# Kernel optimization log

Measured on AMD Instinct MI355X. Metric: run time of the kernel, lower is better.

Reference implementation:

```python
import jax, jax.numpy as jnp
import numpy as np

B, S, H = 512, 100, 768
LAMB = 0.8

def setup_inputs() -> dict:
    key = jax.random.key(0)
    k1, k2, k3, k4 = jax.random.split(key, 4)
    scale = 1.0 / np.sqrt(H)
    return {
        "sent_vec": jax.random.normal(k1, (B, S, H), dtype=jnp.float32),
        "mask_cls": jnp.ones((B, S), dtype=jnp.int32),
        "W_cont": jax.random.normal(k2, (1, H), dtype=jnp.float32) * scale,
        "W_sim": jax.random.normal(k3, (H, H), dtype=jnp.float32) * scale,
        "W_rel": jax.random.normal(k4, (H, H), dtype=jnp.float32) * scale,
        "b_matrix": jnp.zeros((1, 1), dtype=jnp.float32),
    }

def reference(sent_vec, mask_cls, W_cont, W_sim, W_rel, b_matrix):
    # sent_vec: [B,S,H], mask_cls: [B,S] (all ones -> true_dim == S)
    m = mask_cls.astype(sent_vec.dtype)                       # [B,S]
    mask2 = m[:, :, None] * m[:, None, :]                     # mask_my_own [B,S,S]

    # Score_Cont[b,i,j] = W_cont . sent_vec[b,i]
    cont = jnp.einsum('h,bih->bi', W_cont[0], sent_vec)       # [B,S]
    # Score_Sim[b,i,j] = sent_i W_sim sent_j^T, masked
    sim = jnp.einsum('bih,hk,bjk->bij', sent_vec, W_sim, sent_vec) * mask2
    # Score_rel[b,i,j] = sent_i W_rel d_rep, masked
    d_rep = sent_vec.mean(axis=1)                             # [B,H]
    rel = jnp.einsum('bih,hk,bk->bi', sent_vec, W_rel, d_rep) # [B,S]

    q = jax.nn.sigmoid(rel[:, :, None] * mask2 + cont[:, :, None] + sim + b_matrix[0, 0])
    q = q * mask2                                             # [B,S,S]

    # D = diag(column sums of q); q @ D^{-1} divides columns by sum_vec
    sum_vec = q.sum(axis=1)                                   # [B,S]
    qD = q / sum_vec[:, None, :]                              # [B,S,S]

    I = jnp.eye(S, dtype=q.dtype)
    M = I[None, :, :] - LAMB * qD                             # [B,S,S]
    y = jnp.full((B, S, 1), 1.0 / S, dtype=q.dtype)
    # Final_score = (1-lamb) * inv(I - lamb q D^-1) @ y  (solve == inverse@mm)
    score = (1.0 - LAMB) * jnp.linalg.solve(M, y)[:, :, 0]    # [B,S]
    return score
```

## Files before the change

### kernel.cpp

```cpp
#include <hip/hip_runtime.h>
#include <math.h>

#define BB 512
#define SS 100
#define HH 768

typedef __bf16 bf16x8 __attribute__((ext_vector_type(8)));
typedef __bf16 bf16x4 __attribute__((ext_vector_type(4)));
typedef float f32x4 __attribute__((ext_vector_type(4)));
typedef float f32x16 __attribute__((ext_vector_type(16)));

__device__ __forceinline__ void gld16(const void* g, void* l) {
    __builtin_amdgcn_global_load_lds((const __attribute__((address_space(1))) char*)g,
                                     (__attribute__((address_space(3))) char*)l, 16, 0, 0);
}

__global__ __launch_bounds__(256) void k_drep(const float* __restrict__ X,
                                              float* __restrict__ drep) {
    int b = blockIdx.x, g = blockIdx.y;
    int lane = threadIdx.x & 63, w = threadIdx.x >> 6;
    const float4* xb = (const float4*)(X + (size_t)b * SS * HH);
    int c4 = g * 64 + lane;
    float4 s = {0.f, 0.f, 0.f, 0.f};
    for (int r = w; r < SS; r += 4) {
        float4 v = xb[r * 192 + c4];
        s.x += v.x; s.y += v.y; s.z += v.z; s.w += v.w;
    }
    __shared__ float4 red[4][64];
    red[w][lane] = s;
    __syncthreads();
    if (w == 0) {
        float4 a0 = red[0][lane], a1 = red[1][lane], a2 = red[2][lane], a3 = red[3][lane];
        float4 o;
        o.x = (a0.x + a1.x + a2.x + a3.x) * (1.0f / SS);
        o.y = (a0.y + a1.y + a2.y + a3.y) * (1.0f / SS);
        o.z = (a0.z + a1.z + a2.z + a3.z) * (1.0f / SS);
        o.w = (a0.w + a1.w + a2.w + a3.w) * (1.0f / SS);
        ((float4*)(drep + (size_t)b * HH))[c4] = o;
    }
}

__global__ __launch_bounds__(256) void k_gemm_nt(const float* __restrict__ A,
                                                 const float* __restrict__ Bm,
                                                 float* __restrict__ C,
                                                 int N, int K) {
    __shared__ float As[64 * 20];
    __shared__ float Bs[64 * 20];
    int tid = threadIdx.x;
    int ty = tid >> 4, tx = tid & 15;
    int m0 = blockIdx.y * 64, n0 = blockIdx.x * 64;
    int lr = tid >> 2, lc = (tid & 3) * 4;
    float acc[4][4] = {};
    for (int kt = 0; kt < K; kt += 16) {
        *(float4*)(As + lr * 20 + lc) = *(const float4*)(A + (size_t)(m0 + lr) * K + kt + lc);
        *(float4*)(Bs + lr * 20 + lc) = *(const float4*)(Bm + (size_t)(n0 + lr) * K + kt + lc);
        __syncthreads();
        #pragma unroll
        for (int k = 0; k < 16; k += 2) {
            float2 ar[4], br[4];
            #pragma unroll
            for (int ii = 0; ii < 4; ++ii) ar[ii] = *(const float2*)(As + (ty + 16 * ii) * 20 + k);
            #pragma unroll
            for (int jj = 0; jj < 4; ++jj) br[jj] = *(const float2*)(Bs + (tx + 16 * jj) * 20 + k);
            #pragma unroll
            for (int ii = 0; ii < 4; ++ii)
                #pragma unroll
                for (int jj = 0; jj < 4; ++jj)
                    acc[ii][jj] = fmaf(ar[ii].y, br[jj].y, fmaf(ar[ii].x, br[jj].x, acc[ii][jj]));
        }
        __syncthreads();
    }
    #pragma unroll
    for (int ii = 0; ii < 4; ++ii)
        #pragma unroll
        for (int jj = 0; jj < 4; ++jj)
            C[(size_t)(m0 + ty + 16 * ii) * N + n0 + tx + 16 * jj] = acc[ii][jj];
}

__global__ __launch_bounds__(256) void k_splitw(const float* __restrict__ W,
                                                __bf16* __restrict__ th,
                                                __bf16* __restrict__ tl) {
    __shared__ float tile[32][33];
    int bn = blockIdx.x * 32, bk = blockIdx.y * 32;
    int tx = threadIdx.x & 31, ty = threadIdx.x >> 5;
    for (int r = ty; r < 32; r += 8)
        tile[r][tx] = W[(size_t)(bk + r) * HH + bn + tx];
    __syncthreads();
    for (int r = ty; r < 32; r += 8) {
        float v = tile[tx][r];
        __bf16 hv = (__bf16)v;
        size_t idx = (size_t)(bn + r) * HH + bk + tx;
        th[idx] = hv;
        tl[idx] = (__bf16)(v - (float)hv);
    }
}

__global__ __launch_bounds__(512) void k_split_contrel(const float* __restrict__ X,
                                                       const float* __restrict__ Wc,
                                                       const float* __restrict__ tmat,
                                                       const float* __restrict__ bmat,
                                                       __bf16* __restrict__ Xh,
                                                       __bf16* __restrict__ Xl,
                                                       float* __restrict__ avec,
                                                       int b_off) {
    __shared__ float4 u4[192];
    int lb = blockIdx.x, half = blockIdx.y;
    int b = b_off + lb;
    int tid = threadIdx.x, lane = tid & 63, w = tid >> 6;
    for (int c = tid; c < 192; c += 512) {
        float4 wc = ((const float4*)Wc)[c];
        float4 tm = ((const float4*)(tmat + (size_t)b * HH))[c];
        float4 o = {wc.x + tm.x, wc.y + tm.y, wc.z + tm.z, wc.w + tm.w};
        u4[c] = o;
    }
    __syncthreads();
    float b00 = bmat[0];
    const float4* xb = (const float4*)(X + (size_t)b * SS * HH);
    bf16x4* xh4 = (bf16x4*)(Xh + (size_t)lb * SS * HH);
    bf16x4* xl4 = (bf16x4*)(Xl + (size_t)lb * SS * HH);
    int rend = half * 50 + 50;
    for (int r = half * 50 + w; r < rend; r += 8) {
        float s = 0.f;
        #pragma unroll
        for (int cc = 0; cc < 3; ++cc) {
            int c = cc * 64 + lane;
            float4 v = xb[r * 192 + c];
            float4 uu = u4[c];
            s = fmaf(v.x, uu.x, fmaf(v.y, uu.y, fmaf(v.z, uu.z, fmaf(v.w, uu.w, s))));
            bf16x4 hv, lv;
            hv[0] = (__bf16)v.x; lv[0] = (__bf16)(v.x - (float)hv[0]);
            hv[1] = (__bf16)v.y; lv[1] = (__bf16)(v.y - (float)hv[1]);
            hv[2] = (__bf16)v.z; lv[2] = (__bf16)(v.z - (float)hv[2]);
            hv[3] = (__bf16)v.w; lv[3] = (__bf16)(v.w - (float)hv[3]);
            xh4[r * 192 + c] = hv;
            xl4[r * 192 + c] = lv;
        }
        #pragma unroll
        for (int off = 32; off > 0; off >>= 1) s += __shfl_down(s, off);
        if (lane == 0) avec[(size_t)b * SS + r] = s + b00;
    }
}

__global__ __launch_bounds__(256) void k_gemm1_mfma(const __bf16* __restrict__ Ah_g,
                                                    const __bf16* __restrict__ Al_g,
                                                    const __bf16* __restrict__ Bh_g,
                                                    const __bf16* __restrict__ Bl_g,
                                                    __bf16* __restrict__ Yh,
                                                    __bf16* __restrict__ Yl) {
    __shared__ __align__(16) __bf16 lds[2 * 4 * 4096];
    const int tid = threadIdx.x;
    const int wave = tid >> 6, lane = tid & 63;
    const int wy = wave >> 1, wx = wave & 1;
    const int lid = blockIdx.x + 6 * blockIdx.y;
    const int tile = (lid & 7) * 300 + (lid >> 3);
    const size_t m0 = (size_t)(tile / 6) * 128;
    const int n0 = (tile % 6) * 128;

    const int srow = wave * 32 + (lane >> 2);
    const int scol = ((lane & 3) ^ ((lane >> 3) & 3)) * 8;
    const int lds_base = wave * 1024;

    const int arow = wy * 64 + (lane & 31);
    const int brow = wx * 64 + (lane & 31);
    const int sw = (lane >> 1) & 3;

    f32x16 acc[2][2] = {};

    auto stage = [&](int buf, int kt) {
        __bf16* base = lds + buf * 16384;
        const size_t ga0 = (m0 + srow) * HH + kt + scol;
        const size_t ga1 = ga0 + (size_t)16 * HH;
        const size_t gb0 = (size_t)(n0 + srow) * HH + kt + scol;
        const size_t gb1 = gb0 + (size_t)16 * HH;
        gld16(Ah_g + ga0, base + lds_base);
        gld16(Ah_g + ga1, base + lds_base + 512);
        gld16(Al_g + ga0, base + 4096 + lds_base);
        gld16(Al_g + ga1, base + 4096 + lds_base + 512);
        gld16(Bh_g + gb0, base + 8192 + lds_base);
        gld16(Bh_g + gb1, base + 8192 + lds_base + 512);
        gld16(Bl_g + gb0, base + 12288 + lds_base);
        gld16(Bl_g + gb1, base + 12288 + lds_base + 512);
    };
    auto compute = [&](int buf) {
        const __bf16* As_h = lds + buf * 16384;
        const __bf16* As_l = As_h + 4096;
        const __bf16* Bs_h = As_h + 8192;
        const __bf16* Bs_l = As_h + 12288;
        #pragma unroll
        for (int kh = 0; kh < 2; ++kh) {
            const int ko = (((kh << 1) + (lane >> 5)) ^ sw) << 3;
            bf16x8 fah[2], fal[2], fbh[2], fbl[2];
            #pragma unroll
            for (int t = 0; t < 2; ++t) {
                fah[t] = *(const bf16x8*)(As_h + (arow + t * 32) * 32 + ko);
                fal[t] = *(const bf16x8*)(As_l + (arow + t * 32) * 32 + ko);
                fbh[t] = *(const bf16x8*)(Bs_h + (brow + t * 32) * 32 + ko);
                fbl[t] = *(const bf16x8*)(Bs_l + (brow + t * 32) * 32 + ko);
            }
            #pragma unroll
            for (int ti = 0; ti < 2; ++ti)
                #pragma unroll
                for (int tj = 0; tj < 2; ++tj) {
                    acc[ti][tj] = __builtin_amdgcn_mfma_f32_32x32x16_bf16(fal[ti], fbh[tj], acc[ti][tj], 0, 0, 0);
                    acc[ti][tj] = __builtin_amdgcn_mfma_f32_32x32x16_bf16(fah[ti], fbl[tj], acc[ti][tj], 0, 0, 0);
                    acc[ti][tj] = __builtin_amdgcn_mfma_f32_32x32x16_bf16(fah[ti], fbh[tj], acc[ti][tj], 0, 0, 0);
                }
        }
    };

    stage(0, 0);
    int cur = 0;
    for (int kt = 32; kt < HH; kt += 32) {
        stage(cur ^ 1, kt);
        asm volatile("s_waitcnt vmcnt(8)" ::: "memory");
        __builtin_amdgcn_s_barrier();
        compute(cur);
        __builtin_amdgcn_s_barrier();
        cur ^= 1;
    }
    asm volatile("s_waitcnt vmcnt(0)" ::: "memory");
    __builtin_amdgcn_s_barrier();
    compute(cur);

    const int rbase = 4 * (lane >> 5);
    const int colb = lane & 31;
    #pragma unroll
    for (int ti = 0; ti < 2; ++ti) {
        #pragma unroll
        for (int tj = 0; tj < 2; ++tj) {
            int col = n0 + wx * 64 + tj * 32 + colb;
            #pragma unroll
            for (int r = 0; r < 16; ++r) {
                int row = wy * 64 + ti * 32 + (r & 3) + 8 * (r >> 2) + rbase;
                float v = acc[ti][tj][r];
                __bf16 hv = (__bf16)v;
                size_t idx = (m0 + row) * HH + col;
                Yh[idx] = hv;
                Yl[idx] = (__bf16)(v - (float)hv);
            }
        }
    }
}

__global__ __launch_bounds__(256) void k_gemm2_mfma(const __bf16* __restrict__ Yh,
                                                    const __bf16* __restrict__ Yl,
                                                    const __bf16* __restrict__ Xh,
                                                    const __bf16* __restrict__ Xl,
                                                    const float* __restrict__ avec,
                                                    float* __restrict__ q, int b_off) {
    __shared__ __align__(16) __bf16 lds[2 * 4 * 4096];
    __shared__ float av_s[SS];
    const int bl = blockIdx.x;
    const int b = b_off + bl;
    const __bf16* Ah_g = Yh + (size_t)bl * SS * HH;
    const __bf16* Al_g = Yl + (size_t)bl * SS * HH;
    const __bf16* Bh_g = Xh + (size_t)bl * SS * HH;
    const __bf16* Bl_g = Xl + (size_t)bl * SS * HH;
    const int tid = threadIdx.x;
    const int wave = tid >> 6, lane = tid & 63;
    const int wy = wave >> 1, wx = wave & 1;
    if (tid < SS) av_s[tid] = avec[(size_t)b * SS + tid];

    const int srow_raw = wave * 32 + (lane >> 2);
    const int scol = ((lane & 3) ^ ((lane >> 3) & 3)) * 8;
    const int lds_base = wave * 1024;
    const int r0 = srow_raw < SS ? srow_raw : SS - 1;
    const int r1 = (srow_raw + 16) < SS ? (srow_raw + 16) : SS - 1;

    const int arow = wy * 64 + (lane & 31);
    const int brow = wx * 64 + (lane & 31);
    const int sw = (lane >> 1) & 3;

    f32x16 acc[2][2] = {};

    auto stage = [&](int buf, int kt) {
        __bf16* base = lds + buf * 16384;
        const size_t ga0 = (size_t)r0 * HH + kt + scol;
        const size_t ga1 = (size_t)r1 * HH + kt + scol;
        gld16(Ah_g + ga0, base + lds_base);
        gld16(Ah_g + ga1, base + lds_base + 512);
        gld16(Al_g + ga0, base + 4096 + lds_base);
        gld16(Al_g + ga1, base + 4096 + lds_base + 512);
        gld16(Bh_g + ga0, base + 8192 + lds_base);
        gld16(Bh_g + ga1, base + 8192 + lds_base + 512);
        gld16(Bl_g + ga0, base + 12288 + lds_base);
        gld16(Bl_g + ga1, base + 12288 + lds_base + 512);
    };
    auto compute = [&](int buf) {
        const __bf16* As_h = lds + buf * 16384;
        const __bf16* As_l = As_h + 4096;
        const __bf16* Bs_h = As_h + 8192;
        const __bf16* Bs_l = As_h + 12288;
        #pragma unroll
        for (int kh = 0; kh < 2; ++kh) {
            const int ko = (((kh << 1) + (lane >> 5)) ^ sw) << 3;
            bf16x8 fah[2], fal[2], fbh[2], fbl[2];
            #pragma unroll
            for (int t = 0; t < 2; ++t) {
                fah[t] = *(const bf16x8*)(As_h + (arow + t * 32) * 32 + ko);
                fal[t] = *(const bf16x8*)(As_l + (arow + t * 32) * 32 + ko);
                fbh[t] = *(const bf16x8*)(Bs_h + (brow + t * 32) * 32 + ko);
                fbl[t] = *(const bf16x8*)(Bs_l + (brow + t * 32) * 32 + ko);
            }
            #pragma unroll
            for (int ti = 0; ti < 2; ++ti)
                #pragma unroll
                for (int tj = 0; tj < 2; ++tj) {
                    acc[ti][tj] = __builtin_amdgcn_mfma_f32_32x32x16_bf16(fal[ti], fbh[tj], acc[ti][tj], 0, 0, 0);
                    acc[ti][tj] = __builtin_amdgcn_mfma_f32_32x32x16_bf16(fah[ti], fbl[tj], acc[ti][tj], 0, 0, 0);
                    acc[ti][tj] = __builtin_amdgcn_mfma_f32_32x32x16_bf16(fah[ti], fbh[tj], acc[ti][tj], 0, 0, 0);
                }
        }
    };

    stage(0, 0);
    int cur = 0;
    for (int kt = 32; kt < HH; kt += 32) {
        stage(cur ^ 1, kt);
        asm volatile("s_waitcnt vmcnt(8)" ::: "memory");
        __builtin_amdgcn_s_barrier();
        compute(cur);
        __builtin_amdgcn_s_barrier();
        cur ^= 1;
    }
    asm volatile("s_waitcnt vmcnt(0)" ::: "memory");
    __builtin_amdgcn_s_barrier();
    compute(cur);

    float* qb = q + (size_t)b * SS * SS;
    const int rbase = 4 * (lane >> 5);
    const int colb = lane & 31;
    #pragma unroll
    for (int ti = 0; ti < 2; ++ti) {
        #pragma unroll
        for (int tj = 0; tj < 2; ++tj) {
            int j = wx * 64 + tj * 32 + colb;
            if (j >= SS) continue;
            #pragma unroll
            for (int r = 0; r < 16; ++r) {
                int i = wy * 64 + ti * 32 + (r & 3) + 8 * (r >> 2) + rbase;
                if (i >= SS) continue;
                float v = acc[ti][tj][r] + av_s[i];
                qb[(size_t)i * SS + j] = 1.0f / (1.0f + __expf(-v));
            }
        }
    }
}

__global__ __launch_bounds__(128) void k_solve(const float* __restrict__ q,
                                               float* __restrict__ out) {
    __shared__ __align__(16) float m[SS * SS];
    __shared__ __align__(16) float csinv[SS];
    __shared__ __align__(16) float x0[SS], x1[SS];
    int b = blockIdx.x, tid = threadIdx.x;
    const float* qb = q + (size_t)b * SS * SS;
    for (int e4 = tid; e4 < SS * SS / 4; e4 += 128)
        *(float4*)(m + e4 * 4) = *(const float4*)(qb + (size_t)e4 * 4);
    __syncthreads();
    if (tid < SS) {
        float s = 0.f;
        for (int i = 0; i < SS; ++i) s += m[i * SS + tid];
        csinv[tid] = 0.8f / s;
        x0[tid] = 1.0f / SS;
    }
    __syncthreads();
    float4 mreg[25];
    if (tid < SS) {
        #pragma unroll
        for (int j4 = 0; j4 < 25; ++j4) {
            float4 mv = *(const float4*)(m + tid * SS + j4 * 4);
            float4 cv = *(const float4*)(csinv + j4 * 4);
            mreg[j4].x = mv.x * cv.x;
            mreg[j4].y = mv.y * cv.y;
            mreg[j4].z = mv.z * cv.z;
            mreg[j4].w = mv.w * cv.w;
        }
    } else {
        #pragma unroll
        for (int j4 = 0; j4 < 25; ++j4) mreg[j4] = float4{0, 0, 0, 0};
    }
    __syncthreads();
    #pragma unroll 1
    for (int it = 0; it < 56; ++it) {
        const float* xr = (it & 1) ? x1 : x0;
        float* xw = (it & 1) ? x0 : x1;
        if (tid < SS) {
            float sx = 0.f, sy = 0.f, sz = 0.f, sw = 0.f;
            #pragma unroll
            for (int j4 = 0; j4 < 25; ++j4) {
                float4 xv = *(const float4*)(xr + j4 * 4);
                sx = fmaf(mreg[j4].x, xv.x, sx);
                sy = fmaf(mreg[j4].y, xv.y, sy);
                sz = fmaf(mreg[j4].z, xv.z, sz);
                sw = fmaf(mreg[j4].w, xv.w, sw);
            }
            xw[tid] = 0.002f + ((sx + sy) + (sz + sw));
        }
        __syncthreads();
    }
    if (tid < SS) out[(size_t)b * SS + tid] = x0[tid];
}

extern "C" void kernel_launch(void* const* d_in, const int* in_sizes, int n_in,
                              void* d_out, int out_size, void* d_ws, size_t ws_size,
                              hipStream_t stream) {
    (void)in_sizes; (void)n_in; (void)out_size;
    const float* X    = (const float*)d_in[0];
    const float* Wc   = (const float*)d_in[2];
    const float* Wsim = (const float*)d_in[3];
    const float* Wrel = (const float*)d_in[4];
    const float* bmat = (const float*)d_in[5];
    float* out = (float*)d_out;

    char* ws = (char*)d_ws;
    size_t off = 0;
    float*  qbuf = (float*)(ws + off);  off += (size_t)BB * SS * SS * 4;
    float*  drep = (float*)(ws + off);  off += (size_t)BB * HH * 4;
    float*  tmat = (float*)(ws + off);  off += (size_t)BB * HH * 4;
    float*  avec = (float*)(ws + off);  off += (size_t)BB * SS * 4;
    __bf16* Wth  = (__bf16*)(ws + off); off += (size_t)HH * HH * 2;
    __bf16* Wtl  = (__bf16*)(ws + off); off += (size_t)HH * HH * 2;

    int CB = 512;
    while (CB > 128 && off + 4 * (size_t)CB * SS * HH * 2 > ws_size) CB >>= 1;
    size_t xsz = (size_t)CB * SS * HH * 2;
    __bf16* Xh = (__bf16*)(ws + off); off += xsz;
    __bf16* Xl = (__bf16*)(ws + off); off += xsz;
    __bf16* Yh = (__bf16*)(ws + off); off += xsz;
    __bf16* Yl = (__bf16*)(ws + off); off += xsz;

    k_drep<<<dim3(BB, 3), 256, 0, stream>>>(X, drep);
    k_gemm_nt<<<dim3(HH / 64, BB / 64), 256, 0, stream>>>(drep, Wrel, tmat, HH, HH);
    k_splitw<<<dim3(HH / 32, HH / 32), 256, 0, stream>>>(Wsim, Wth, Wtl);

    for (int c = 0; c < BB; c += CB) {
        k_split_contrel<<<dim3(CB, 2), 512, 0, stream>>>(X + (size_t)c * SS * HH, Wc, tmat, bmat, Xh, Xl, avec, c);
        k_gemm1_mfma<<<dim3(HH / 128, CB * SS / 128), 256, 0, stream>>>(Xh, Xl, Wth, Wtl, Yh, Yl);
        k_gemm2_mfma<<<CB, 256, 0, stream>>>(Yh, Yl, Xh, Xl, avec, qbuf, c);
    }
    k_solve<<<BB, 128, 0, stream>>>(qbuf, out);
}
```

Before: 697.4 us.

## Enlarge gemm1 tile to 256x256 with 8 waves and XCD-aware tile mapping

Grows the split-bf16 GEMM1 block tile from 128x128 with 4 waves to 256x256 with 8 waves, each wave now computing a 128x64 sub-tile. This raises operand reuse per LDS load and halves global traffic per output. It also replaces the fixed 2D grid swizzle with a 1D grid whose tiles are assigned contiguously per XCD, to improve L2 locality. In exchange it uses twice the LDS (128KB double-buffered) and more accumulator registers, which lowers occupancy and gives fewer blocks (600) to spread across the CUs.

```diff
diff --git a/kernel.cpp b/kernel.cpp
--- a/kernel.cpp
+++ b/kernel.cpp
@@ -141,64 +141,70 @@
     }
 }
 
-__global__ __launch_bounds__(256) void k_gemm1_mfma(const __bf16* __restrict__ Ah_g,
+__global__ __launch_bounds__(512) void k_gemm1_mfma(const __bf16* __restrict__ Ah_g,
                                                     const __bf16* __restrict__ Al_g,
                                                     const __bf16* __restrict__ Bh_g,
                                                     const __bf16* __restrict__ Bl_g,
                                                     __bf16* __restrict__ Yh,
                                                     __bf16* __restrict__ Yl) {
-    __shared__ __align__(16) __bf16 lds[2 * 4 * 4096];
+    __shared__ __align__(16) __bf16 lds[2 * 32768];
     const int tid = threadIdx.x;
     const int wave = tid >> 6, lane = tid & 63;
-    const int wy = wave >> 1, wx = wave & 1;
-    const int lid = blockIdx.x + 6 * blockIdx.y;
-    const int tile = (lid & 7) * 300 + (lid >> 3);
-    const size_t m0 = (size_t)(tile / 6) * 128;
-    const int n0 = (tile % 6) * 128;
-
-    const int srow = wave * 32 + (lane >> 2);
+    const int wy = wave >> 2, wx = wave & 3;
+    const int nwg = gridDim.x;
+    const int lid = blockIdx.x;
+    const int q8 = nwg >> 3, r8 = nwg & 7;
+    const int xcd = lid & 7, idx = lid >> 3;
+    const int tile = (xcd < r8 ? xcd * (q8 + 1) : r8 * (q8 + 1) + (xcd - r8) * q8) + idx;
+    const size_t m0 = (size_t)(tile / 3) * 256;
+    const int n0 = (tile % 3) * 256;
+
+    const int srow = tid >> 2;
     const int scol = ((lane & 3) ^ ((lane >> 3) & 3)) * 8;
-    const int lds_base = wave * 1024;
-
-    const int arow = wy * 64 + (lane & 31);
+    const int wbase = wave * 512;
+
+    const int arow = wy * 128 + (lane & 31);
     const int brow = wx * 64 + (lane & 31);
     const int sw = (lane >> 1) & 3;
 
-    f32x16 acc[2][2] = {};
+    f32x16 acc[4][2] = {};
 
     auto stage = [&](int buf, int kt) {
-        __bf16* base = lds + buf * 16384;
+        __bf16* base = lds + buf * 32768;
         const size_t ga0 = (m0 + srow) * HH + kt + scol;
-        const size_t ga1 = ga0 + (size_t)16 * HH;
+        const size_t ga1 = ga0 + (size_t)128 * HH;
         const size_t gb0 = (size_t)(n0 + srow) * HH + kt + scol;
-        const size_t gb1 = gb0 + (size_t)16 * HH;
-        gld16(Ah_g + ga0, base + lds_base);
-        gld16(Ah_g + ga1, base + lds_base + 512);
-        gld16(Al_g + ga0, base + 4096 + lds_base);
-        gld16(Al_g + ga1, base + 4096 + lds_base + 512);
-        gld16(Bh_g + gb0, base + 8192 + lds_base);
-        gld16(Bh_g + gb1, base + 8192 + lds_base + 512);
-        gld16(Bl_g + gb0, base + 12288 + lds_base);
-        gld16(Bl_g + gb1, base + 12288 + lds_base + 512);
+        const size_t gb1 = gb0 + (size_t)128 * HH;
+        gld16(Ah_g + ga0, base + wbase);
+        gld16(Ah_g + ga1, base + 4096 + wbase);
+        gld16(Al_g + ga0, base + 8192 + wbase);
+        gld16(Al_g + ga1, base + 12288 + wbase);
+        gld16(Bh_g + gb0, base + 16384 + wbase);
+        gld16(Bh_g + gb1, base + 20480 + wbase);
+        gld16(Bl_g + gb0, base + 24576 + wbase);
+        gld16(Bl_g + gb1, base + 28672 + wbase);
     };
     auto compute = [&](int buf) {
-        const __bf16* As_h = lds + buf * 16384;
-        const __bf16* As_l = As_h + 4096;
-        const __bf16* Bs_h = As_h + 8192;
-        const __bf16* Bs_l = As_h + 12288;
+        const __bf16* Ah_s = lds + buf * 32768;
+        const __bf16* Al_s = Ah_s + 8192;
+        const __bf16* Bh_s = Ah_s + 16384;
+        const __bf16* Bl_s = Ah_s + 24576;
         #pragma unroll
         for (int kh = 0; kh < 2; ++kh) {
             const int ko = (((kh << 1) + (lane >> 5)) ^ sw) << 3;
-            bf16x8 fah[2], fal[2], fbh[2], fbl[2];
+            bf16x8 fah[4], fal[4], fbh[2], fbl[2];
+            #pragma unroll
+            for (int t = 0; t < 4; ++t) {
+                fah[t] = *(const bf16x8*)(Ah_s + (arow + t * 32) * 32 + ko);
+                fal[t] = *(const bf16x8*)(Al_s + (arow + t * 32) * 32 + ko);
+            }
             #pragma unroll
             for (int t = 0; t < 2; ++t) {
-                fah[t] = *(const bf16x8*)(As_h + (arow + t * 32) * 32 + ko);
-                fal[t] = *(const bf16x8*)(As_l + (arow + t * 32) * 32 + ko);
-                fbh[t] = *(const bf16x8*)(Bs_h + (brow + t * 32) * 32 + ko);
-                fbl[t] = *(const bf16x8*)(Bs_l + (brow + t * 32) * 32 + ko);
-            }
-            #pragma unroll
-            for (int ti = 0; ti < 2; ++ti)
+                fbh[t] = *(const bf16x8*)(Bh_s + (brow + t * 32) * 32 + ko);
+                fbl[t] = *(const bf16x8*)(Bl_s + (brow + t * 32) * 32 + ko);
+            }
+            #pragma unroll
+            for (int ti = 0; ti < 4; ++ti)
                 #pragma unroll
                 for (int tj = 0; tj < 2; ++tj) {
                     acc[ti][tj] = __builtin_amdgcn_mfma_f32_32x32x16_bf16(fal[ti], fbh[tj], acc[ti][tj], 0, 0, 0);
@@ -225,13 +231,13 @@
     const int rbase = 4 * (lane >> 5);
     const int colb = lane & 31;
     #pragma unroll
-    for (int ti = 0; ti < 2; ++ti) {
+    for (int ti = 0; ti < 4; ++ti) {
         #pragma unroll
         for (int tj = 0; tj < 2; ++tj) {
             int col = n0 + wx * 64 + tj * 32 + colb;
             #pragma unroll
             for (int r = 0; r < 16; ++r) {
-                int row = wy * 64 + ti * 32 + (r & 3) + 8 * (r >> 2) + rbase;
+                int row = wy * 128 + ti * 32 + (r & 3) + 8 * (r >> 2) + rbase;
                 float v = acc[ti][tj][r];
                 __bf16 hv = (__bf16)v;
                 size_t idx = (m0 + row) * HH + col;
@@ -435,7 +441,8 @@
 
     for (int c = 0; c < BB; c += CB) {
         k_split_contrel<<<dim3(CB, 2), 512, 0, stream>>>(X + (size_t)c * SS * HH, Wc, tmat, bmat, Xh, Xl, avec, c);
-        k_gemm1_mfma<<<dim3(HH / 128, CB * SS / 128), 256, 0, stream>>>(Xh, Xl, Wth, Wtl, Yh, Yl);
+        int nblk1 = (CB * SS / 256) * (HH / 256);
+        k_gemm1_mfma<<<nblk1, 512, 0, stream>>>(Xh, Xl, Wth, Wtl, Yh, Yl);
         k_gemm2_mfma<<<CB, 256, 0, stream>>>(Yh, Yl, Xh, Xl, avec, qbuf, c);
     }
     k_solve<<<BB, 128, 0, stream>>>(qbuf, out);
```

Result: no change. 709.6 us (+1.8%).

## Split staging of A and B, interleave B prefetch mid-compute, add setprio and generic XCD remap

Applied to the files above, without the earlier changes.

Both MFMA GEMM kernels now issue the next tile's A loads before the barrier and delay the B loads until after the first k-half of compute, so each wait only covers four outstanding loads. MFMA blocks are wrapped in s_setprio to favour the compute waves. The final tile is folded into the loop. gemm1 moves to a 1D grid with an XCD-aware tile remap that handles grid sizes not divisible by 8, where the old code hardcoded 300 tiles per XCD. The goal is better load/compute overlap and correct L2 locality for any chunk size. The risk is that exposing B-load latency inside the iteration could stall compute if the loads land late.

```diff
diff --git a/kernel.cpp b/kernel.cpp
--- a/kernel.cpp
+++ b/kernel.cpp
@@ -151,8 +151,11 @@
     const int tid = threadIdx.x;
     const int wave = tid >> 6, lane = tid & 63;
     const int wy = wave >> 1, wx = wave & 1;
-    const int lid = blockIdx.x + 6 * blockIdx.y;
-    const int tile = (lid & 7) * 300 + (lid >> 3);
+    const int nwg = gridDim.x;
+    const int lid = blockIdx.x;
+    const int q8 = nwg >> 3, r8 = nwg & 7;
+    const int xcd = lid & 7, sidx = lid >> 3;
+    const int tile = (xcd < r8 ? xcd * (q8 + 1) : r8 * (q8 + 1) + (xcd - r8) * q8) + sidx;
     const size_t m0 = (size_t)(tile / 6) * 128;
     const int n0 = (tile % 6) * 128;
 
@@ -166,61 +169,68 @@
 
     f32x16 acc[2][2] = {};
 
-    auto stage = [&](int buf, int kt) {
+    auto stageA = [&](int buf, int kt) {
         __bf16* base = lds + buf * 16384;
         const size_t ga0 = (m0 + srow) * HH + kt + scol;
         const size_t ga1 = ga0 + (size_t)16 * HH;
-        const size_t gb0 = (size_t)(n0 + srow) * HH + kt + scol;
-        const size_t gb1 = gb0 + (size_t)16 * HH;
         gld16(Ah_g + ga0, base + lds_base);
         gld16(Ah_g + ga1, base + lds_base + 512);
         gld16(Al_g + ga0, base + 4096 + lds_base);
         gld16(Al_g + ga1, base + 4096 + lds_base + 512);
+    };
+    auto stageB = [&](int buf, int kt) {
+        __bf16* base = lds + buf * 16384;
+        const size_t gb0 = (size_t)(n0 + srow) * HH + kt + scol;
+        const size_t gb1 = gb0 + (size_t)16 * HH;
         gld16(Bh_g + gb0, base + 8192 + lds_base);
         gld16(Bh_g + gb1, base + 8192 + lds_base + 512);
         gld16(Bl_g + gb0, base + 12288 + lds_base);
         gld16(Bl_g + gb1, base + 12288 + lds_base + 512);
     };
-    auto compute = [&](int buf) {
+    auto compute_kh = [&](int buf, int kh) {
         const __bf16* As_h = lds + buf * 16384;
         const __bf16* As_l = As_h + 4096;
         const __bf16* Bs_h = As_h + 8192;
         const __bf16* Bs_l = As_h + 12288;
-        #pragma unroll
-        for (int kh = 0; kh < 2; ++kh) {
-            const int ko = (((kh << 1) + (lane >> 5)) ^ sw) << 3;
-            bf16x8 fah[2], fal[2], fbh[2], fbl[2];
-            #pragma unroll
-            for (int t = 0; t < 2; ++t) {
-                fah[t] = *(const bf16x8*)(As_h + (arow + t * 32) * 32 + ko);
-                fal[t] = *(const bf16x8*)(As_l + (arow + t * 32) * 32 + ko);
-                fbh[t] = *(const bf16x8*)(Bs_h + (brow + t * 32) * 32 + ko);
-                fbl[t] = *(const bf16x8*)(Bs_l + (brow + t * 32) * 32 + ko);
+        const int ko = (((kh << 1) + (lane >> 5)) ^ sw) << 3;
+        bf16x8 fah[2], fal[2], fbh[2], fbl[2];
+        #pragma unroll
+        for (int t = 0; t < 2; ++t) {
+            fah[t] = *(const bf16x8*)(As_h + (arow + t * 32) * 32 + ko);
+            fal[t] = *(const bf16x8*)(As_l + (arow + t * 32) * 32 + ko);
+            fbh[t] = *(const bf16x8*)(Bs_h + (brow + t * 32) * 32 + ko);
+            fbl[t] = *(const bf16x8*)(Bs_l + (brow + t * 32) * 32 + ko);
+        }
+        __builtin_amdgcn_s_setprio(1);
+        #pragma unroll
+        for (int ti = 0; ti < 2; ++ti)
+            #pragma unroll
+            for (int tj = 0; tj < 2; ++tj) {
+                acc[ti][tj] = __builtin_amdgcn_mfma_f32_32x32x16_bf16(fal[ti], fbh[tj], acc[ti][tj], 0, 0, 0);
+                acc[ti][tj] = __builtin_amdgcn_mfma_f32_32x32x16_bf16(fah[ti], fbl[tj], acc[ti][tj], 0, 0, 0);
+                acc[ti][tj] = __builtin_amdgcn_mfma_f32_32x32x16_bf16(fah[ti], fbh[tj], acc[ti][tj], 0, 0, 0);
             }
-            #pragma unroll
-            for (int ti = 0; ti < 2; ++ti)
-                #pragma unroll
-                for (int tj = 0; tj < 2; ++tj) {
-                    acc[ti][tj] = __builtin_amdgcn_mfma_f32_32x32x16_bf16(fal[ti], fbh[tj], acc[ti][tj], 0, 0, 0);
-                    acc[ti][tj] = __builtin_amdgcn_mfma_f32_32x32x16_bf16(fah[ti], fbl[tj], acc[ti][tj], 0, 0, 0);
-                    acc[ti][tj] = __builtin_amdgcn_mfma_f32_32x32x16_bf16(fah[ti], fbh[tj], acc[ti][tj], 0, 0, 0);
-                }
-        }
-    };
-
-    stage(0, 0);
+        __builtin_amdgcn_s_setprio(0);
+    };
+
+    stageA(0, 0);
+    stageB(0, 0);
     int cur = 0;
-    for (int kt = 32; kt < HH; kt += 32) {
-        stage(cur ^ 1, kt);
-        asm volatile("s_waitcnt vmcnt(8)" ::: "memory");
+    for (int i = 0; i < HH / 32; ++i) {
+        const int nkt = (i + 1) * 32;
+        if (nkt < HH) {
+            stageA(cur ^ 1, nkt);
+            asm volatile("s_waitcnt vmcnt(4)" ::: "memory");
+        } else {
+            asm volatile("s_waitcnt vmcnt(0)" ::: "memory");
+        }
         __builtin_amdgcn_s_barrier();
-        compute(cur);
+        compute_kh(cur, 0);
+        if (nkt < HH) stageB(cur ^ 1, nkt);
+        compute_kh(cur, 1);
         __builtin_amdgcn_s_barrier();
         cur ^= 1;
     }
-    asm volatile("s_waitcnt vmcnt(0)" ::: "memory");
-    __builtin_amdgcn_s_barrier();
-    compute(cur);
 
     const int rbase = 4 * (lane >> 5);
     const int colb = lane & 31;
@@ -273,7 +283,7 @@
 
     f32x16 acc[2][2] = {};
 
-    auto stage = [&](int buf, int kt) {
+    auto stageA = [&](int buf, int kt) {
         __bf16* base = lds + buf * 16384;
         const size_t ga0 = (size_t)r0 * HH + kt + scol;
         const size_t ga1 = (size_t)r1 * HH + kt + scol;
@@ -281,51 +291,60 @@
         gld16(Ah_g + ga1, base + lds_base + 512);
         gld16(Al_g + ga0, base + 4096 + lds_base);
         gld16(Al_g + ga1, base + 4096 + lds_base + 512);
+    };
+    auto stageB = [&](int buf, int kt) {
+        __bf16* base = lds + buf * 16384;
+        const size_t ga0 = (size_t)r0 * HH + kt + scol;
+        const size_t ga1 = (size_t)r1 * HH + kt + scol;
         gld16(Bh_g + ga0, base + 8192 + lds_base);
         gld16(Bh_g + ga1, base + 8192 + lds_base + 512);
         gld16(Bl_g + ga0, base + 12288 + lds_base);
         gld16(Bl_g + ga1, base + 12288 + lds_base + 512);
     };
-    auto compute = [&](int buf) {
+    auto compute_kh = [&](int buf, int kh) {
         const __bf16* As_h = lds + buf * 16384;
         const __bf16* As_l = As_h + 4096;
         const __bf16* Bs_h = As_h + 8192;
         const __bf16* Bs_l = As_h + 12288;
-        #pragma unroll
-        for (int kh = 0; kh < 2; ++kh) {
-            const int ko = (((kh << 1) + (lane >> 5)) ^ sw) << 3;
-            bf16x8 fah[2], fal[2], fbh[2], fbl[2];
-            #pragma unroll
-            for (int t = 0; t < 2; ++t) {
-                fah[t] = *(const bf16x8*)(As_h + (arow + t * 32) * 32 + ko);
-                fal[t] = *(const bf16x8*)(As_l + (arow + t * 32) * 32 + ko);
-                fbh[t] = *(const bf16x8*)(Bs_h + (brow + t * 32) * 32 + ko);
-                fbl[t] = *(const bf16x8*)(Bs_l + (brow + t * 32) * 32 + ko);
+        const int ko = (((kh << 1) + (lane >> 5)) ^ sw) << 3;
+        bf16x8 fah[2], fal[2], fbh[2], fbl[2];
+        #pragma unroll
+        for (int t = 0; t < 2; ++t) {
+            fah[t] = *(const bf16x8*)(As_h + (arow + t * 32) * 32 + ko);
+            fal[t] = *(const bf16x8*)(As_l + (arow + t * 32) * 32 + ko);
+            fbh[t] = *(const bf16x8*)(Bs_h + (brow + t * 32) * 32 + ko);
+            fbl[t] = *(const bf16x8*)(Bs_l + (brow + t * 32) * 32 + ko);
+        }
+        __builtin_amdgcn_s_setprio(1);
+        #pragma unroll
+        for (int ti = 0; ti < 2; ++ti)
+            #pragma unroll
+            for (int tj = 0; tj < 2; ++tj) {
+                acc[ti][tj] = __builtin_amdgcn_mfma_f32_32x32x16_bf16(fal[ti], fbh[tj], acc[ti][tj], 0, 0, 0);
+                acc[ti][tj] = __builtin_amdgcn_mfma_f32_32x32x16_bf16(fah[ti], fbl[tj], acc[ti][tj], 0, 0, 0);
+                acc[ti][tj] = __builtin_amdgcn_mfma_f32_32x32x16_bf16(fah[ti], fbh[tj], acc[ti][tj], 0, 0, 0);
             }
-            #pragma unroll
-            for (int ti = 0; ti < 2; ++ti)
-                #pragma unroll
-                for (int tj = 0; tj < 2; ++tj) {
-                    acc[ti][tj] = __builtin_amdgcn_mfma_f32_32x32x16_bf16(fal[ti], fbh[tj], acc[ti][tj], 0, 0, 0);
-                    acc[ti][tj] = __builtin_amdgcn_mfma_f32_32x32x16_bf16(fah[ti], fbl[tj], acc[ti][tj], 0, 0, 0);
-                    acc[ti][tj] = __builtin_amdgcn_mfma_f32_32x32x16_bf16(fah[ti], fbh[tj], acc[ti][tj], 0, 0, 0);
-                }
-        }
-    };
-
-    stage(0, 0);
+        __builtin_amdgcn_s_setprio(0);
+    };
+
+    stageA(0, 0);
+    stageB(0, 0);
     int cur = 0;
-    for (int kt = 32; kt < HH; kt += 32) {
-        stage(cur ^ 1, kt);
-        asm volatile("s_waitcnt vmcnt(8)" ::: "memory");
+    for (int i = 0; i < HH / 32; ++i) {
+        const int nkt = (i + 1) * 32;
+        if (nkt < HH) {
+            stageA(cur ^ 1, nkt);
+            asm volatile("s_waitcnt vmcnt(4)" ::: "memory");
+        } else {
+            asm volatile("s_waitcnt vmcnt(0)" ::: "memory");
+        }
         __builtin_amdgcn_s_barrier();
-        compute(cur);
+        compute_kh(cur, 0);
+        if (nkt < HH) stageB(cur ^ 1, nkt);
+        compute_kh(cur, 1);
         __builtin_amdgcn_s_barrier();
         cur ^= 1;
     }
-    asm volatile("s_waitcnt vmcnt(0)" ::: "memory");
-    __builtin_amdgcn_s_barrier();
-    compute(cur);
 
     float* qb = q + (size_t)b * SS * SS;
     const int rbase = 4 * (lane >> 5);
@@ -435,7 +454,7 @@
 
     for (int c = 0; c < BB; c += CB) {
         k_split_contrel<<<dim3(CB, 2), 512, 0, stream>>>(X + (size_t)c * SS * HH, Wc, tmat, bmat, Xh, Xl, avec, c);
-        k_gemm1_mfma<<<dim3(HH / 128, CB * SS / 128), 256, 0, stream>>>(Xh, Xl, Wth, Wtl, Yh, Yl);
+        k_gemm1_mfma<<<CB * SS / 128 * (HH / 128), 256, 0, stream>>>(Xh, Xl, Wth, Wtl, Yh, Yl);
         k_gemm2_mfma<<<CB, 256, 0, stream>>>(Yh, Yl, Xh, Xl, avec, qbuf, c);
     }
     k_solve<<<BB, 128, 0, stream>>>(qbuf, out);
```

New measurement: 706.3 us. No clear change (+1.3%).
